# Kernel tuning notes

Measured on AMD Instinct MI355X. Metric: run time of the kernel, lower is better.

## Reference

```python
import jax, jax.numpy as jnp
import numpy as np

# DREAMPlace IDXST_IDCT (a.k.a. idsct2): y[u,v] = sum_p sum_q x[p,q] * sin(pi*p*(u+0.5)/M) * cos(pi*q*(v+0.5)/N)
# i.e. IDXST (inverse discrete sine transform, DST-III-like, unnormalized) along the M axis
# and IDCT (DCT-III-like, unnormalized, full weight on k=0) along the N axis.
# Computed with the classic 2N-padded FFT trick using the precomputed twiddles
# expk[k] = exp(-1j*pi*k/(2N)) stored as [N,2] (real, imag), matching precompute_expk.

def _idxt_spectrum(x, expk):
    """F[u] = sum_k x[k] * exp(-1j*pi*k*(2u+1)/(2N)), along last axis.
    Re(F) is the IDCT sum (cos), -Im(F) is the IDXST sum (sin)."""
    N = x.shape[-1]
    c = (x * expk[..., 0]) + 1j * (x * expk[..., 1])  # x[k] * exp(-j*pi*k/(2N))
    z = jnp.concatenate([c, jnp.zeros_like(c)], axis=-1)  # zero-pad to 2N
    return jnp.fft.fft(z, axis=-1)[..., :N]


def idct_1d(x, expk):
    # y[u] = sum_k x[k] cos(pi*k*(2u+1)/(2N))
    return _idxt_spectrum(x, expk).real


def idxst_1d(x, expk):
    # y[u] = sum_k x[k] sin(pi*k*(2u+1)/(2N))
    return -_idxt_spectrum(x, expk).imag


def _make_expk(L):
    k = jnp.arange(L, dtype=jnp.float32) * (np.pi / (2.0 * L))
    return jnp.stack([jnp.cos(k), -jnp.sin(k)], axis=-1)  # exp(-j*pi*k/(2L))


def setup_inputs() -> dict:
    M, N = 4096, 4096
    key = jax.random.key(0)
    x = jax.random.normal(key, (M, N), dtype=jnp.float32)
    return {"x": x, "expkM": _make_expk(M), "expkN": _make_expk(N)}


def reference(x, expkM, expkN):
    # IDCT along the last dim (N), then IDXST along the second-to-last dim (M):
    # idxst(idct(x)^T)^T
    t = idct_1d(x, expkN)                                        # [M, N]
    y = idxst_1d(t.swapaxes(-2, -1), expkM).swapaxes(-2, -1)     # [M, N]
    return y
```

## Files before the change

### kernel.cpp

```cpp
#include <hip/hip_runtime.h>
#include <hip/hip_bf16.h>
#include <stdint.h>
#include <cmath>


typedef __attribute__((ext_vector_type(4))) float f32x4;
typedef __attribute__((ext_vector_type(8))) unsigned short u16x8;
typedef __attribute__((ext_vector_type(8))) __bf16 bf16x8;

__device__ __forceinline__ unsigned short f2bf(float f) {
  union { float f; unsigned u; } v; v.f = f;
  unsigned u = v.u + 0x7fffu + ((v.u >> 16) & 1u);
  return (unsigned short)(u >> 16);
}

__device__ __forceinline__ void gen_half(int idx, u16x8* Pe, u16x8* Po,
                                         int isSin, int jshift, int jmask,
                                         unsigned mask4L, float sc) {
  int i = idx >> jshift;
  int jb = (idx & jmask) * 8;
  unsigned tp = 2u * (unsigned)i + 1u;
  unsigned re = (2u * (unsigned)jb * tp) & mask4L;
  unsigned ro = (re + tp) & mask4L;
  unsigned step = (2u * tp) & mask4L;
  u16x8 pe, po;
#pragma unroll
  for (int t = 0; t < 8; t++) {
    float se_, ce_, so_, co_;
    __sincosf((float)re * sc, &se_, &ce_);
    __sincosf((float)ro * sc, &so_, &co_);
    pe[t] = f2bf(isSin ? se_ : ce_);
    po[t] = f2bf(isSin ? so_ : co_);
    re = (re + step) & mask4L;
    ro = (ro + step) & mask4L;
  }
  Pe[idx] = pe;
  Po[idx] = po;
}

__global__ void prep_kernel(const f32x4* __restrict__ x, u16x8* __restrict__ xe,
                            u16x8* __restrict__ xo, u16x8* __restrict__ Ce,
                            u16x8* __restrict__ Co, u16x8* __restrict__ Se,
                            u16x8* __restrict__ So, int nConvBlocks,
                            int nGenNBlocks, int jshiftN, int jmaskN,
                            unsigned mask4N, float scN, int jshiftM, int jmaskM,
                            unsigned mask4M, float scM) {
  int b = blockIdx.x;
  if (b < nConvBlocks) {
    int idx = b * 256 + threadIdx.x;
    f32x4 a = x[4 * idx], bb = x[4 * idx + 1], c = x[4 * idx + 2],
          d = x[4 * idx + 3];
    u16x8 e, o;
    e[0] = f2bf(a[0]);  o[0] = f2bf(a[1]);  e[1] = f2bf(a[2]);  o[1] = f2bf(a[3]);
    e[2] = f2bf(bb[0]); o[2] = f2bf(bb[1]); e[3] = f2bf(bb[2]); o[3] = f2bf(bb[3]);
    e[4] = f2bf(c[0]);  o[4] = f2bf(c[1]);  e[5] = f2bf(c[2]);  o[5] = f2bf(c[3]);
    e[6] = f2bf(d[0]);  o[6] = f2bf(d[1]);  e[7] = f2bf(d[2]);  o[7] = f2bf(d[3]);
    xe[idx] = e;
    xo[idx] = o;
  } else if (b < nConvBlocks + nGenNBlocks) {
    int idx = (b - nConvBlocks) * 256 + threadIdx.x;
    gen_half(idx, Ce, Co, 0, jshiftN, jmaskN, mask4N, scN);
  } else {
    int idx = (b - nConvBlocks - nGenNBlocks) * 256 + threadIdx.x;
    gen_half(idx, Se, So, 1, jshiftM, jmaskM, mask4M, scM);
  }
}

template <int STAGE>
__global__ __launch_bounds__(256, 2) void fused_gemm_kernel(
    const unsigned short* __restrict__ Ae,
    const unsigned short* __restrict__ Ao,
    const unsigned short* __restrict__ Be,
    const unsigned short* __restrict__ Bo,
    unsigned short* __restrict__ out0, unsigned short* __restrict__ out1,
    int outStride, int K, int Lfull) {
  __shared__ unsigned short As[128 * 64];
  __shared__ unsigned short Bs[128 * 64];

  const int tid = threadIdx.x;
  const int m0 = blockIdx.y * 128;
  const int n0 = blockIdx.x * 128;

  const int wave = tid >> 6;
  const int lane = tid & 63;
  const int wm = (wave & 1) * 64;
  const int wn = (wave >> 1) * 64;
  const int l16 = lane & 15;
  const int quad = lane >> 4;

  const int lrow = lane >> 3;
  const int lsw = ((lane & 7) ^ lrow) * 8;
  unsigned short* Al[4];
  unsigned short* Bl[4];
#pragma unroll
  for (int t = 0; t < 4; t++) {
    int ch = wave + 4 * t;
    Al[t] = As + ch * 512;
    Bl[t] = Bs + ch * 512;
  }
  const int swz = (quad ^ (l16 & 7)) * 8;

  f32x4 accE[4][4], accO[4][4];

  auto kloop = [&](const unsigned short* __restrict__ A,
                   const unsigned short* __restrict__ Bt,
                   f32x4 (&acc)[4][4]) {
#pragma unroll
    for (int i = 0; i < 4; i++)
#pragma unroll
      for (int j = 0; j < 4; j++) acc[i][j] = f32x4{0.f, 0.f, 0.f, 0.f};

    const unsigned short* Ag[4];
    const unsigned short* Bg[4];
#pragma unroll
    for (int t = 0; t < 4; t++) {
      int ch = wave + 4 * t;
      Ag[t] = A + (size_t)(m0 + 8 * ch + lrow) * K + lsw;
      Bg[t] = Bt + (size_t)(n0 + 8 * ch + lrow) * K + lsw;
    }

    for (int k0 = 0; k0 < K; k0 += 64) {
#pragma unroll
      for (int t = 0; t < 4; t++) {
        __builtin_amdgcn_global_load_lds(
            (const __attribute__((address_space(1))) void*)(Ag[t] + k0),
            (__attribute__((address_space(3))) void*)Al[t], 16, 0, 0);
        __builtin_amdgcn_global_load_lds(
            (const __attribute__((address_space(1))) void*)(Bg[t] + k0),
            (__attribute__((address_space(3))) void*)Bl[t], 16, 0, 0);
      }
      __syncthreads();

#pragma unroll
      for (int h = 0; h < 2; h++) {
        const int so = swz ^ (h * 32);
        bf16x8 af[4], bfr[4];
#pragma unroll
        for (int i = 0; i < 4; i++) {
          af[i]  = *(const bf16x8*)(As + (wm + i * 16 + l16) * 64 + so);
          bfr[i] = *(const bf16x8*)(Bs + (wn + i * 16 + l16) * 64 + so);
        }
#pragma unroll
        for (int i = 0; i < 4; i++)
#pragma unroll
          for (int j = 0; j < 4; j++)
            acc[i][j] = __builtin_amdgcn_mfma_f32_16x16x32_bf16(
                af[i], bfr[j], acc[i][j], 0, 0, 0);
      }
      __syncthreads();
    }
  };

  kloop(Ae, Be, accE);
  kloop(Ao, Bo, accO);

#pragma unroll
  for (int i = 0; i < 4; i++) {
#pragma unroll
    for (int j = 0; j < 4; j++) {
      int n = n0 + wn + j * 16 + l16;
      int mb = m0 + wm + i * 16 + quad * 4;
#pragma unroll
      for (int r = 0; r < 4; r++) {
        float e = accE[i][j][r];
        float o = accO[i][j][r];
        int m = mb + r;
        if (STAGE == 1) {
          unsigned short* mat = (n & 1) ? out1 : out0;
          int c = n >> 1;
          mat[(size_t)m * outStride + c] = f2bf(e + o);
          mat[(size_t)(Lfull - 1 - m) * outStride + c] = f2bf(e - o);
        } else {
          float* y = (float*)out0;
          y[(size_t)m * outStride + n] = e + o;
          y[(size_t)(Lfull - 1 - m) * outStride + n] = o - e;
        }
      }
    }
  }
}

extern "C" void kernel_launch(void* const* d_in, const int* in_sizes, int n_in,
                              void* d_out, int out_size, void* d_ws,
                              size_t ws_size, hipStream_t stream) {
  const float* x = (const float*)d_in[0];
  const int M = in_sizes[1] / 2;
  const int N = in_sizes[2] / 2;
  const size_t MN = (size_t)M * N;

  unsigned short* ws = (unsigned short*)d_ws;
  unsigned short* xe = ws;
  unsigned short* xo = ws + MN / 2;
  unsigned short* Ce = ws + MN;
  unsigned short* Co = ws + MN + MN / 4;
  unsigned short* Se = ws + MN * 3 / 2;
  unsigned short* So = ws + MN * 7 / 4;
  unsigned short* tTe = ws + MN * 2;
  unsigned short* tTo = ws + MN * 5 / 2;

  int shiftN = 0; while ((1 << shiftN) < N) shiftN++;
  int shiftM = 0; while ((1 << shiftM) < M) shiftM++;

  int nConvBlocks = (int)(MN / 16 / 256);
  int nGenNBlocks = (N / 2) * (N / 2) / 8 / 256;
  int nGenMBlocks = (M / 2) * (M / 2) / 8 / 256;
  prep_kernel<<<nConvBlocks + nGenNBlocks + nGenMBlocks, 256, 0, stream>>>(
      (const f32x4*)x, (u16x8*)xe, (u16x8*)xo, (u16x8*)Ce, (u16x8*)Co,
      (u16x8*)Se, (u16x8*)So, nConvBlocks, nGenNBlocks, shiftN - 4,
      (N / 16) - 1, (unsigned)(4 * N - 1),
      (float)(3.14159265358979323846 / (2.0 * N)), shiftM - 4, (M / 16) - 1,
      (unsigned)(4 * M - 1), (float)(3.14159265358979323846 / (2.0 * M)));

  fused_gemm_kernel<1><<<dim3(M / 128, (N / 2) / 128), 256, 0, stream>>>(
      Ce, Co, xe, xo, tTe, tTo, M / 2, N / 2, N);

  fused_gemm_kernel<2><<<dim3(N / 128, (M / 2) / 128), 256, 0, stream>>>(
      Se, So, tTe, tTo, (unsigned short*)d_out, nullptr, N, M / 2, M);
}
```

Before: 283.8 us.

## Double-buffer even/odd GEMM phases, widen tile to 128x256, swizzle block order

The two sequential even/odd K-loops are merged into one loop that ping-pongs between separate LDS buffers. Loads for one half are issued while MFMAs run on the other, so global-to-LDS latency overlaps with compute. The block tile grows to 128x256 with 512 threads, which raises reuse of the A operand. The workgroup index is remapped in groups of 8 to improve L2 locality. The cost is 96KB of LDS per block, which may limit occupancy to one block per CU.

```diff
diff --git a/kernel.cpp b/kernel.cpp
--- a/kernel.cpp
+++ b/kernel.cpp
@@ -67,92 +67,101 @@
 }
 
 template <int STAGE>
-__global__ __launch_bounds__(256, 2) void fused_gemm_kernel(
+__global__ __launch_bounds__(512, 2) void fused_gemm_kernel(
     const unsigned short* __restrict__ Ae,
     const unsigned short* __restrict__ Ao,
     const unsigned short* __restrict__ Be,
     const unsigned short* __restrict__ Bo,
     unsigned short* __restrict__ out0, unsigned short* __restrict__ out1,
     int outStride, int K, int Lfull) {
-  __shared__ unsigned short As[128 * 64];
-  __shared__ unsigned short Bs[128 * 64];
+  __shared__ unsigned short AsE[128 * 64];
+  __shared__ unsigned short BsE[256 * 64];
+  __shared__ unsigned short AsO[128 * 64];
+  __shared__ unsigned short BsO[256 * 64];
 
   const int tid = threadIdx.x;
-  const int m0 = blockIdx.y * 128;
-  const int n0 = blockIdx.x * 128;
+
+  const int nwg = gridDim.x * gridDim.y;
+  const int lin = blockIdx.y * gridDim.x + blockIdx.x;
+  int swb = lin;
+  if ((nwg & 7) == 0) swb = (lin & 7) * (nwg >> 3) + (lin >> 3);
+  const int m0 = (swb / gridDim.x) * 128;
+  const int n0 = (swb % gridDim.x) * 256;
 
   const int wave = tid >> 6;
   const int lane = tid & 63;
-  const int wm = (wave & 1) * 64;
-  const int wn = (wave >> 1) * 64;
+  const int wm = (wave >> 2) * 64;
+  const int wn = (wave & 3) * 64;
   const int l16 = lane & 15;
   const int quad = lane >> 4;
+  const int swz = (quad ^ (l16 & 7)) * 8;
 
   const int lrow = lane >> 3;
   const int lsw = ((lane & 7) ^ lrow) * 8;
-  unsigned short* Al[4];
-  unsigned short* Bl[4];
-#pragma unroll
-  for (int t = 0; t < 4; t++) {
-    int ch = wave + 4 * t;
-    Al[t] = As + ch * 512;
-    Bl[t] = Bs + ch * 512;
-  }
-  const int swz = (quad ^ (l16 & 7)) * 8;
+
+  auto stage = [&](const unsigned short* __restrict__ A,
+                   const unsigned short* __restrict__ B, unsigned short* As,
+                   unsigned short* Bs, int k0) {
+    const unsigned short* Ap =
+        A + (size_t)(m0 + 8 * wave + lrow) * K + lsw + k0;
+    const unsigned short* Bp =
+        B + (size_t)(n0 + 8 * wave + lrow) * K + lsw + k0;
+    unsigned short* Adst = As + wave * 512;
+    unsigned short* Bdst = Bs + wave * 512;
+#define GLL(src, dst)                                                        \
+  __builtin_amdgcn_global_load_lds(                                          \
+      (const __attribute__((address_space(1))) void*)(src),                  \
+      (__attribute__((address_space(3))) void*)(dst), 16, 0, 0)
+    GLL(Ap, Adst);
+    GLL(Ap + (size_t)64 * K, Adst + 4096);
+    GLL(Bp, Bdst);
+    GLL(Bp + (size_t)64 * K, Bdst + 4096);
+    GLL(Bp + (size_t)128 * K, Bdst + 8192);
+    GLL(Bp + (size_t)192 * K, Bdst + 12288);
+#undef GLL
+  };
 
   f32x4 accE[4][4], accO[4][4];
-
-  auto kloop = [&](const unsigned short* __restrict__ A,
-                   const unsigned short* __restrict__ Bt,
+#pragma unroll
+  for (int i = 0; i < 4; i++)
+#pragma unroll
+    for (int j = 0; j < 4; j++) {
+      accE[i][j] = f32x4{0.f, 0.f, 0.f, 0.f};
+      accO[i][j] = f32x4{0.f, 0.f, 0.f, 0.f};
+    }
+
+  auto phase = [&](const unsigned short* As, const unsigned short* Bs,
                    f32x4 (&acc)[4][4]) {
 #pragma unroll
-    for (int i = 0; i < 4; i++)
-#pragma unroll
-      for (int j = 0; j < 4; j++) acc[i][j] = f32x4{0.f, 0.f, 0.f, 0.f};
-
-    const unsigned short* Ag[4];
-    const unsigned short* Bg[4];
-#pragma unroll
-    for (int t = 0; t < 4; t++) {
-      int ch = wave + 4 * t;
-      Ag[t] = A + (size_t)(m0 + 8 * ch + lrow) * K + lsw;
-      Bg[t] = Bt + (size_t)(n0 + 8 * ch + lrow) * K + lsw;
-    }
-
-    for (int k0 = 0; k0 < K; k0 += 64) {
-#pragma unroll
-      for (int t = 0; t < 4; t++) {
-        __builtin_amdgcn_global_load_lds(
-            (const __attribute__((address_space(1))) void*)(Ag[t] + k0),
-            (__attribute__((address_space(3))) void*)Al[t], 16, 0, 0);
-        __builtin_amdgcn_global_load_lds(
-            (const __attribute__((address_space(1))) void*)(Bg[t] + k0),
-            (__attribute__((address_space(3))) void*)Bl[t], 16, 0, 0);
-      }
-      __syncthreads();
-
-#pragma unroll
-      for (int h = 0; h < 2; h++) {
-        const int so = swz ^ (h * 32);
-        bf16x8 af[4], bfr[4];
-#pragma unroll
-        for (int i = 0; i < 4; i++) {
-          af[i]  = *(const bf16x8*)(As + (wm + i * 16 + l16) * 64 + so);
-          bfr[i] = *(const bf16x8*)(Bs + (wn + i * 16 + l16) * 64 + so);
-        }
-#pragma unroll
-        for (int i = 0; i < 4; i++)
-#pragma unroll
-          for (int j = 0; j < 4; j++)
-            acc[i][j] = __builtin_amdgcn_mfma_f32_16x16x32_bf16(
-                af[i], bfr[j], acc[i][j], 0, 0, 0);
-      }
-      __syncthreads();
+    for (int h = 0; h < 2; h++) {
+      const int so = swz ^ (h * 32);
+      bf16x8 af[4], bfr[4];
+#pragma unroll
+      for (int i = 0; i < 4; i++)
+        af[i] = *(const bf16x8*)(As + (wm + i * 16 + l16) * 64 + so);
+#pragma unroll
+      for (int j = 0; j < 4; j++)
+        bfr[j] = *(const bf16x8*)(Bs + (wn + j * 16 + l16) * 64 + so);
+#pragma unroll
+      for (int i = 0; i < 4; i++)
+#pragma unroll
+        for (int j = 0; j < 4; j++)
+          acc[i][j] = __builtin_amdgcn_mfma_f32_16x16x32_bf16(
+              af[i], bfr[j], acc[i][j], 0, 0, 0);
     }
   };
 
-  kloop(Ae, Be, accE);
-  kloop(Ao, Bo, accO);
+  stage(Ae, Be, AsE, BsE, 0);
+  __syncthreads();
+
+  for (int k0 = 0; k0 < K; k0 += 64) {
+    stage(Ao, Bo, AsO, BsO, k0);
+    phase(AsE, BsE, accE);
+    __syncthreads();
+    if (k0 + 64 < K) stage(Ae, Be, AsE, BsE, k0 + 64);
+    phase(AsO, BsO, accO);
+    __syncthreads();
+  }
 
 #pragma unroll
   for (int i = 0; i < 4; i++) {
@@ -211,9 +220,9 @@
       (float)(3.14159265358979323846 / (2.0 * N)), shiftM - 4, (M / 16) - 1,
       (unsigned)(4 * M - 1), (float)(3.14159265358979323846 / (2.0 * M)));
 
-  fused_gemm_kernel<1><<<dim3(M / 128, (N / 2) / 128), 256, 0, stream>>>(
+  fused_gemm_kernel<1><<<dim3(M / 256, (N / 2) / 128), 512, 0, stream>>>(
       Ce, Co, xe, xo, tTe, tTo, M / 2, N / 2, N);
 
-  fused_gemm_kernel<2><<<dim3(N / 128, (M / 2) / 128), 256, 0, stream>>>(
+  fused_gemm_kernel<2><<<dim3(N / 256, (M / 2) / 128), 512, 0, stream>>>(
       Se, So, tTe, tTo, (unsigned short*)d_out, nullptr, N, M / 2, M);
 }
```

Measured after the change: 270.4 us. 1.05x faster.
